# Kernel tuning notes

Hardware: AMD Instinct MI355X
Metric: run time of the kernel (lower is better)

Reference implementation:

```python
import math
import jax, jax.numpy as jnp
import numpy as np

L_LAYERS, H, D, DV, DM, LMAX, V = 4, 16, 1024, 64, 4096, 1024, 32000


def setup_inputs() -> dict:
    key = jax.random.key(0)
    ks = iter(jax.random.split(key, 40))
    def rn(shape, s=0.02):
        return jax.random.normal(next(ks), shape, jnp.float32) * s
    x_ids = jax.random.randint(next(ks), (LMAX,), 0, V)
    return dict(
        x_ids=x_ids,
        word_emb=rn((V, D)), pos_emb=rn((LMAX, D)),
        Wq=rn((L_LAYERS, H, D, D)), bq=jnp.zeros((L_LAYERS, H, D), jnp.float32),
        Wk=rn((L_LAYERS, H, D, D)), bk=jnp.zeros((L_LAYERS, H, D), jnp.float32),
        Wv=rn((L_LAYERS, H, D, DV)), bv=jnp.zeros((L_LAYERS, H, DV), jnp.float32),
        Wo=rn((L_LAYERS, H * DV, D)), bo=jnp.zeros((L_LAYERS, D), jnp.float32),
        g1=rn((L_LAYERS, D), 0.01), b1=rn((L_LAYERS, D), 0.01),
        g2=rn((L_LAYERS, D), 0.01), b2=rn((L_LAYERS, D), 0.01),
        W1=rn((L_LAYERS, D, DM)), bm1=jnp.zeros((L_LAYERS, DM), jnp.float32),
        W2=rn((L_LAYERS, DM, D)), bm2=jnp.zeros((L_LAYERS, D), jnp.float32),
        gf=rn((D,), 0.01), bf=rn((D,), 0.01),
        Wu=rn((D, V)), bu=jnp.zeros((V,), jnp.float32),
    )


def _ln(x, g, b):
    # original normalizes each row over the full embedding vector (biased std)
    mu = jnp.mean(x, axis=-1, keepdims=True)
    sd = jnp.sqrt(jnp.mean((x - mu) ** 2, axis=-1, keepdims=True))
    return g * (x - mu) / sd + b


def reference(x_ids, word_emb, pos_emb, Wq, bq, Wk, bk, Wv, bv, Wo, bo,
              g1, b1, g2, b2, W1, bm1, W2, bm2, gf, bf, Wu, bu):
    x = word_emb[x_ids] + pos_emb[jnp.arange(LMAX)]          # (LMAX, D)
    mask = jnp.tril(jnp.ones((LMAX, LMAX), bool))
    scale = 1.0 / math.sqrt(D)                               # d_attn = d_e
    for l in range(L_LAYERS):
        xn = _ln(x, g1[l], b1[l])
        q = jnp.einsum('ld,hde->hle', xn, Wq[l]) + bq[l][:, None, :]
        k = jnp.einsum('ld,hde->hle', xn, Wk[l]) + bk[l][:, None, :]
        v = jnp.einsum('ld,hdv->hlv', xn, Wv[l]) + bv[l][:, None, :]
        s = jnp.einsum('hqe,hke->hqk', q, k)                 # (H, LMAX, LMAX)
        s = jnp.where(mask, s, -jnp.inf)
        a = jax.nn.softmax(s * scale, axis=-1)
        o = jnp.einsum('hqk,hkv->hqv', a, v)                 # (H, LMAX, DV)
        # faithful reproduction of MHAttention's OVERLAPPING slice writes:
        # head h writes columns [h, h+DV), later heads overwrite earlier ones
        y = jnp.zeros((LMAX, H * DV), x.dtype)
        for h in range(H):
            y = y.at[:, h:h + DV].set(o[h])
        x = x + y @ Wo[l] + bo[l]
        xn2 = _ln(x, g2[l], b2[l])
        # x + act_layer(xn2) where act_layer(z) = z + mlp2(gelu(mlp1(z)))
        x = x + xn2 + jax.nn.gelu(xn2 @ W1[l] + bm1[l]) @ W2[l] + bm2[l]
    x = _ln(x, gf, bf)
    return jax.nn.softmax(x @ Wu + bu, axis=-1)              # (LMAX, V)
```

## Files before the change

kernel.cpp:

```cpp
#include <hip/hip_runtime.h>

typedef __bf16 bf16_t;
typedef __bf16 bf16x8 __attribute__((ext_vector_type(8)));
typedef float f32x4 __attribute__((ext_vector_type(4)));
typedef unsigned int u32;

#define SEQ    1024
#define DEMB   1024
#define NHEAD  16
#define DVDIM  64
#define DMLP   4096
#define NVOCAB 32000
#define NLAYER 4

typedef const __attribute__((address_space(1))) void gas_t;
typedef __attribute__((address_space(3))) void las_t;

__device__ __forceinline__ void gload_lds16(const void* g, void* l) {
  __builtin_amdgcn_global_load_lds((gas_t*)g, (las_t*)l, 16, 0, 0);
}

union PackU { bf16_t h[2]; u32 u; };
union B4U  { uint2 u; bf16_t h[4]; };

__device__ __forceinline__ float blockSum(float v, float* red) {
  #pragma unroll
  for (int o = 32; o > 0; o >>= 1) v += __shfl_down(v, o, 64);
  __syncthreads();
  if ((threadIdx.x & 63) == 0) red[threadIdx.x >> 6] = v;
  __syncthreads();
  return (red[0] + red[1]) + (red[2] + red[3]);
}
__device__ __forceinline__ float blockMax(float v, float* red) {
  #pragma unroll
  for (int o = 32; o > 0; o >>= 1) v = fmaxf(v, __shfl_down(v, o, 64));
  __syncthreads();
  if ((threadIdx.x & 63) == 0) red[threadIdx.x >> 6] = v;
  __syncthreads();
  return fmaxf(fmaxf(red[0], red[1]), fmaxf(red[2], red[3]));
}

__device__ __forceinline__ void ln_body(float4 v, const float* __restrict__ g,
                                        const float* __restrict__ b,
                                        bf16_t* __restrict__ xn, int row, int t,
                                        float* red, float* xupd_row) {
  float mu = blockSum(v.x + v.y + v.z + v.w, red) * (1.0f / DEMB);
  float dx = v.x - mu, dy = v.y - mu, dz = v.z - mu, dw = v.w - mu;
  float var = blockSum(dx * dx + dy * dy + dz * dz + dw * dw, red) * (1.0f / DEMB);
  float inv = 1.0f / sqrtf(var);
  float4 gv = *(const float4*)(g + t * 4);
  float4 bv = *(const float4*)(b + t * 4);
  float o0 = gv.x * dx * inv + bv.x;
  float o1 = gv.y * dy * inv + bv.y;
  float o2 = gv.z * dz * inv + bv.z;
  float o3 = gv.w * dw * inv + bv.w;
  PackU p0, p1;
  p0.h[0] = (bf16_t)o0; p0.h[1] = (bf16_t)o1;
  p1.h[0] = (bf16_t)o2; p1.h[1] = (bf16_t)o3;
  uint2 st; st.x = p0.u; st.y = p1.u;
  *(uint2*)(xn + (long)row * DEMB + t * 4) = st;
  if (xupd_row) {
    float4 nv; nv.x = v.x + o0; nv.y = v.y + o1; nv.z = v.z + o2; nv.w = v.w + o3;
    *(float4*)(xupd_row + t * 4) = nv;
  }
}

__global__ void __launch_bounds__(256)
embedln_k(const int* __restrict__ ids, const float* __restrict__ we,
          const float* __restrict__ pe, const float* __restrict__ g,
          const float* __restrict__ b, float* __restrict__ x,
          bf16_t* __restrict__ xn) {
  __shared__ float red[4];
  const int row = blockIdx.x, t = threadIdx.x;
  const long id = ids[row];
  float4 a = *(const float4*)(we + id * (long)DEMB + t * 4);
  float4 p = *(const float4*)(pe + (long)row * DEMB + t * 4);
  float4 v; v.x = a.x + p.x; v.y = a.y + p.y; v.z = a.z + p.z; v.w = a.w + p.w;
  *(float4*)(x + (long)row * DEMB + t * 4) = v;
  ln_body(v, g, b, xn, row, t, red, nullptr);
}

__global__ void __launch_bounds__(256)
ln_k(const float* __restrict__ x, const float* __restrict__ g,
     const float* __restrict__ b, bf16_t* __restrict__ xn,
     float* __restrict__ xupd) {
  __shared__ float red[4];
  const int row = blockIdx.x, t = threadIdx.x;
  float4 v = *(const float4*)(x + (long)row * DEMB + t * 4);
  ln_body(v, g, b, xn, row, t, red, xupd ? xupd + (long)row * DEMB : nullptr);
}

__global__ void __launch_bounds__(256)
redln_k(const float* __restrict__ P, const float* __restrict__ bm2,
        float* __restrict__ X, const float* __restrict__ g,
        const float* __restrict__ b, bf16_t* __restrict__ xn) {
  __shared__ float red[4];
  const int row = blockIdx.x, t = threadIdx.x;
  const long i = (long)row * 1024 + t * 4;
  float4 x = *(float4*)(X + i);
  #pragma unroll
  for (int z = 0; z < 4; ++z) {
    float4 p = *(const float4*)(P + (long)z * 1048576 + i);
    x.x += p.x; x.y += p.y; x.z += p.z; x.w += p.w;
  }
  float4 bb = *(const float4*)(bm2 + t * 4);
  x.x += bb.x; x.y += bb.y; x.z += bb.z; x.w += bb.w;
  *(float4*)(X + i) = x;
  ln_body(x, g, b, xn, row, t, red, nullptr);
}

__global__ void biaszyb_k(const float* __restrict__ bq, const float* __restrict__ bk,
                          float* __restrict__ out, bf16_t* __restrict__ y) {
  const int z = blockIdx.x, t = threadIdx.x;
  if (z < 128) {
    const int l = z >> 5, i = z & 31;
    const float* src = (i < NHEAD) ? (bq + (long)(l * NHEAD + i) * DEMB)
                                   : (bk + (long)(l * NHEAD + i - NHEAD) * DEMB);
    *(float4*)(out + (long)z * DEMB + t * 4) = *(const float4*)(src + t * 4);
  } else {
    *(uint4*)((char*)y + ((long)(z - 128) * 256 + t) * 16) = uint4{0, 0, 0, 0};
  }
}

__device__ __forceinline__ void tconv_tile(const float* __restrict__ ip,
                                           bf16_t* __restrict__ op,
                                           int R, int C, int rx, int ry,
                                           float (*tf)[65]) {
  const int c0 = rx * 64, r0 = ry * 128;
  const int t = threadIdx.x;
  #pragma unroll
  for (int p = 0; p < 8; ++p) {
    const int i = p * 256 + t;
    const int r = i >> 4, c4 = (i & 15) * 4;
    const float4 v = *(const float4*)(ip + (long)(r0 + r) * C + (c0 + c4));
    *(float4*)&tf[r][c4] = v;
  }
  __syncthreads();
  const int nn = t >> 2;
  const int seg = t & 3;
  #pragma unroll
  for (int q2 = 0; q2 < 4; ++q2) {
    u32 w[4];
    #pragma unroll
    for (int q = 0; q < 4; ++q) {
      const int row = seg * 32 + q2 * 8 + 2 * q;
      PackU u;
      u.h[0] = (bf16_t)tf[row][nn];
      u.h[1] = (bf16_t)tf[row + 1][nn];
      w[q] = u.u;
    }
    *(uint4*)(op + (long)(c0 + nn) * R + (r0 + seg * 32 + q2 * 8)) = *(uint4*)&w[0];
  }
}

__global__ void __launch_bounds__(256)
tconvall_k(const float* __restrict__ Wq, const float* __restrict__ Wk,
           const float* __restrict__ Wv, const float* __restrict__ Wo,
           const float* __restrict__ W1, const float* __restrict__ W2,
           const float* __restrict__ Wu,
           bf16_t* __restrict__ WTqk, bf16_t* __restrict__ WTv,
           bf16_t* __restrict__ WTo, bf16_t* __restrict__ WT1,
           bf16_t* __restrict__ WT2, bf16_t* __restrict__ WTu) {
  __shared__ float tf[128][65];
  const long DD = (long)DEMB * DEMB;
  const int b = blockIdx.x;
  const float* ip; bf16_t* op; int R, C, rx, ry;
  if (b < 16384) {
    const int z = b >> 7, rem = b & 127; ry = rem >> 4; rx = rem & 15;
    R = 1024; C = 1024;
    const int l = z >> 5, i = z & 31;
    ip = (i < NHEAD) ? (Wq + (long)(l * NHEAD + i) * DD)
                     : (Wk + (long)(l * NHEAD + i - NHEAD) * DD);
    op = WTqk + (long)z * DD;
  } else if (b < 16896) {
    const int idx = b - 16384; const int z = idx >> 3; ry = idx & 7; rx = 0;
    R = 1024; C = 64;
    ip = Wv + (long)z * 65536; op = WTv + (long)z * 65536;
  } else if (b < 16960) {
    const int idx = b - 16896; const int z = idx >> 4; ry = 0; rx = idx & 15;
    R = 128; C = 1024;
    ip = Wo + (long)z * DD; op = WTo + (long)z * 131072;
  } else if (b < 19008) {
    const int idx = b - 16960; const int z = idx >> 9, rem = idx & 511;
    ry = rem >> 6; rx = rem & 63;
    R = 1024; C = 4096;
    ip = W1 + (long)z * 4194304; op = WT1 + (long)z * 4194304;
  } else if (b < 21056) {
    const int idx = b - 19008; const int z = idx >> 9, rem = idx & 511;
    ry = rem >> 4; rx = rem & 15;
    R = 4096; C = 1024;
    ip = W2 + (long)z * 4194304; op = WT2 + (long)z * 4194304;
  } else {
    const int idx = b - 21056; ry = idx / 500; rx = idx - ry * 500;
    R = 1024; C = 32000;
    ip = Wu; op = WTu;
  }
  tconv_tile(ip, op, R, C, rx, ry, tf);
}

template<int MODE, int BN, bool CAUSAL, bool TRIMK>
__global__ void __launch_bounds__(256)
gemm_k(const bf16_t* __restrict__ A, const bf16_t* __restrict__ B,
       const float* __restrict__ bias, void* __restrict__ Cv,
       int M, int N, int K, int lda, int ldb,
       long aB, long bB, long cB, int biasB) {
  __shared__ bf16_t lsA[128 * 32];
  __shared__ bf16_t lsB[BN * 32];

  const int t = threadIdx.x;
  const int bz = blockIdx.z;
  const int m0 = blockIdx.y * 128;
  const int n0 = blockIdx.x * BN;
  if (CAUSAL && n0 > m0 + 127) return;

  const bf16_t* Ap = A + (long)bz * aB;
  const bf16_t* Bp = B + (long)bz * bB;
  const int kEnd = TRIMK ? min(K, m0 + 128) : K;

  constexpr int NS = BN / 32;
  const int lane = t & 63;
  const int wid = t >> 6;
  const int wr = (wid >> 1) * 64;
  const int wc = (wid & 1) * (BN / 2);
  const int fr = lane & 15, fg = lane >> 4;
  const int srow = lane >> 2;
  const int skc  = (lane & 3) * 8;

  f32x4 acc[4][NS] = {};

  for (int k0 = 0; k0 < kEnd; k0 += 32) {
    if (k0) __syncthreads();
    #pragma unroll
    for (int i = 0; i < 2; ++i) {
      const int seg = wid * 2 + i;
      gload_lds16(Ap + (long)(m0 + seg * 16 + srow) * lda + (k0 + skc),
                  lsA + seg * 512);
    }
    if (BN == 128) {
      #pragma unroll
      for (int i = 0; i < 2; ++i) {
        const int seg = wid * 2 + i;
        gload_lds16(Bp + (long)(n0 + seg * 16 + srow) * ldb + (k0 + skc),
                    lsB + seg * 512);
      }
    } else {
      gload_lds16(Bp + (long)(n0 + wid * 16 + srow) * ldb + (k0 + skc),
                  lsB + wid * 512);
    }
    __syncthreads();

    bf16x8 af[4], bfv[NS];
    #pragma unroll
    for (int ms = 0; ms < 4; ++ms)
      af[ms] = *(const bf16x8*)(lsA + (wr + ms * 16 + fr) * 32 + fg * 8);
    #pragma unroll
    for (int ns = 0; ns < NS; ++ns)
      bfv[ns] = *(const bf16x8*)(lsB + (wc + ns * 16 + fr) * 32 + fg * 8);
    #pragma unroll
    for (int ms = 0; ms < 4; ++ms)
      #pragma unroll
      for (int ns = 0; ns < NS; ++ns)
        acc[ms][ns] = __builtin_amdgcn_mfma_f32_16x16x32_bf16(
            af[ms], bfv[ns], acc[ms][ns], 0, 0, 0);
  }

  #pragma unroll
  for (int ms = 0; ms < 4; ++ms) {
    #pragma unroll
    for (int ns = 0; ns < NS; ++ns) {
      const int col = n0 + wc + ns * 16 + fr;
      const float bvv = bias ? bias[(long)bz * biasB + col] : 0.0f;
      #pragma unroll
      for (int r = 0; r < 4; ++r) {
        const int row = m0 + wr + ms * 16 + fg * 4 + r;
        float v = acc[ms][ns][r] + bvv;
        if (MODE == 1) {
          ((float*)Cv)[(long)bz * cB + (long)row * N + col] += v;
        } else if (MODE == 2) {
          ((float*)Cv)[(long)bz * cB + (long)row * N + col] = v;
        } else {
          float gl = 0.5f * v * (1.0f + tanhf(0.7978845608028654f * (v + 0.044715f * v * v * v)));
          ((bf16_t*)Cv)[(long)bz * cB + (long)row * N + col] = (bf16_t)gl;
        }
      }
    }
  }
}

#define GPHASE(buf, mh, nh, STAGE, VM) do {                                            \
  bf16x8 af[4][2], bfv[2][2];                                                          \
  _Pragma("unroll") for (int mf = 0; mf < 4; ++mf) {                                   \
    const int r = wm * 128 + ((mh) * 4 + mf) * 16 + (lane & 15);                       \
    _Pragma("unroll") for (int ks = 0; ks < 2; ++ks) {                                 \
      const int slot = ks * 4 + (lane >> 4);                                           \
      af[mf][ks] = *(const bf16x8*)(lds + (buf) * 32768 + r * 64 +                     \
                                    ((slot ^ (r & 7)) << 3)); } }                      \
  _Pragma("unroll") for (int nf = 0; nf < 2; ++nf) {                                   \
    const int r = wn * 64 + ((nh) * 2 + nf) * 16 + (lane & 15);                        \
    _Pragma("unroll") for (int ks = 0; ks < 2; ++ks) {                                 \
      const int slot = ks * 4 + (lane >> 4);                                           \
      bfv[nf][ks] = *(const bf16x8*)(lds + (buf) * 32768 + 16384 + r * 64 +            \
                                     ((slot ^ (r & 7)) << 3)); } }                     \
  STAGE;                                                                               \
  __builtin_amdgcn_s_barrier();                                                        \
  asm volatile("s_waitcnt lgkmcnt(0)" ::: "memory");                                   \
  __builtin_amdgcn_sched_barrier(0);                                                   \
  __builtin_amdgcn_s_setprio(1);                                                       \
  _Pragma("unroll") for (int mf = 0; mf < 4; ++mf)                                     \
    _Pragma("unroll") for (int nf = 0; nf < 2; ++nf)                                   \
      _Pragma("unroll") for (int ks = 0; ks < 2; ++ks)                                 \
        acc[(mh) * 4 + mf][(nh) * 2 + nf] = __builtin_amdgcn_mfma_f32_16x16x32_bf16(   \
            af[mf][ks], bfv[nf][ks], acc[(mh) * 4 + mf][(nh) * 2 + nf], 0, 0, 0);      \
  __builtin_amdgcn_s_setprio(0);                                                       \
  VM;                                                                                  \
  __builtin_amdgcn_s_barrier();                                                        \
} while (0)

template<int MODE, bool CAUSAL, int VZ>
__global__ void __launch_bounds__(512, 1)
gemm256_k(const bf16_t* __restrict__ A, const bf16_t* __restrict__ B,
          const float* __restrict__ bias, void* __restrict__ Cv,
          int M, int N, int K, long aB, long bB, long cB, int biasB,
          const bf16_t* __restrict__ A2, const bf16_t* __restrict__ B2,
          const float* __restrict__ bias2, bf16_t* __restrict__ Cv2) {
  __shared__ bf16_t lds[65536];

  const int t = threadIdx.x;
  const int lane = t & 63, w = t >> 6;
  const int wm = w >> 2, wn = w & 3;
  const int bz = blockIdx.z;
  const int m0 = blockIdx.y * 256, n0 = blockIdx.x * 256;
  const bool vm = (VZ >= 0) && (bz == VZ);
  if (CAUSAL && !vm && n0 > m0 + 255) return;

  const bf16_t* Ap = vm ? A2 : A + (long)bz * aB;
  const bf16_t* Bp = vm ? B2 : B + (long)bz * bB;
  const int NT = K >> 6;

  f32x4 acc[8][4] = {};

  auto stA = [&](int half, int kt, int buf) {
    #pragma unroll
    for (int rr = 0; rr < 2; ++rr) {
      const int rw0 = rr * 64 + w * 8;
      const int row0 = ((rw0 >> 6) << 7) | (half << 6) | (rw0 & 63);
      const int r = row0 + (lane >> 3);
      const int slot = lane & 7;
      gload_lds16(Ap + (long)(m0 + r) * K + (kt << 6) + ((slot ^ (r & 7)) << 3),
                  lds + buf * 32768 + row0 * 64);
    }
  };
  auto stB = [&](int half, int kt, int buf) {
    #pragma unroll
    for (int rr = 0; rr < 2; ++rr) {
      const int rw0 = rr * 64 + w * 8;
      const int row0 = ((rw0 >> 5) << 6) | (half << 5) | (rw0 & 31);
      const int r = row0 + (lane >> 3);
      const int slot = lane & 7;
      gload_lds16(Bp + (long)(n0 + r) * K + (kt << 6) + ((slot ^ (r & 7)) << 3),
                  lds + buf * 32768 + 16384 + row0 * 64);
    }
  };

  stB(0, 0, 0); stA(0, 0, 0); stA(1, 0, 0); stB(1, 0, 0);
  stB(0, 1, 1); stA(0, 1, 1);
  asm volatile("s_waitcnt vmcnt(4)" ::: "memory");
  __builtin_amdgcn_s_barrier();

  for (int it = 0; it < (NT >> 1); ++it) {
    const int tt = it * 2;
    const int s1 = min(tt + 1, NT - 1);
    const int s2 = min(tt + 2, NT - 1);
    const int s3 = min(tt + 3, NT - 1);
    GPHASE(0, 0, 0, { stA(1, s1, 1); }, );
    GPHASE(0, 1, 0, { stB(1, s1, 1); }, );
    GPHASE(0, 0, 1, { stB(0, s2, 0); }, );
    GPHASE(0, 1, 1, { stA(0, s2, 0); }, asm volatile("s_waitcnt vmcnt(4)" ::: "memory"));
    GPHASE(1, 0, 0, { stA(1, s2, 0); }, );
    GPHASE(1, 1, 0, { stB(1, s2, 0); }, );
    GPHASE(1, 0, 1, { stB(0, s3, 1); }, );
    GPHASE(1, 1, 1, { stA(0, s3, 1); }, asm volatile("s_waitcnt vmcnt(4)" ::: "memory"));
  }
  asm volatile("s_waitcnt vmcnt(0)" ::: "memory");

  #pragma unroll
  for (int mf = 0; mf < 8; ++mf) {
    #pragma unroll
    for (int nf = 0; nf < 4; ++nf) {
      const int col = n0 + wn * 64 + nf * 16 + (lane & 15);
      const int row0 = m0 + wm * 128 + mf * 16 + (lane >> 4) * 4;
      if (vm) {
        const float bvv = bias2[col];
        PackU p0, p1;
        p0.h[0] = (bf16_t)(acc[mf][nf][0] + bvv);
        p0.h[1] = (bf16_t)(acc[mf][nf][1] + bvv);
        p1.h[0] = (bf16_t)(acc[mf][nf][2] + bvv);
        p1.h[1] = (bf16_t)(acc[mf][nf][3] + bvv);
        uint2 st; st.x = p0.u; st.y = p1.u;
        *(uint2*)(Cv2 + (long)col * M + row0) = st;
      } else {
        const float bvv = bias ? bias[(long)bz * biasB + col] : 0.0f;
        #pragma unroll
        for (int r = 0; r < 4; ++r) {
          const float v = acc[mf][nf][r] + bvv;
          if (MODE == 0)
            ((bf16_t*)Cv)[(long)bz * cB + (long)(row0 + r) * N + col] = (bf16_t)v;
          else
            ((float*)Cv)[(long)bz * cB + (long)(row0 + r) * N + col] = v;
        }
      }
    }
  }
}

__global__ void __launch_bounds__(256)
smax_k(const bf16_t* __restrict__ s, const bf16_t* __restrict__ V,
       bf16_t* __restrict__ Yb) {
  __shared__ float red[4];
  __shared__ float pl[1024];
  __shared__ float rcol[4][64];
  const int q = blockIdx.x, h = blockIdx.y, t = threadIdx.x;
  const bf16_t* sr = s + ((long)h * SEQ + q) * SEQ;
  const int L = q + 1;
  const float scale = 0.03125f;
  B4U b; b.u = *(const uint2*)(sr + t * 4);
  float x[4];
  float m = -1e30f;
  #pragma unroll
  for (int j = 0; j < 4; ++j) {
    x[j] = (float)b.h[j] * scale;
    if (t * 4 + j < L) m = fmaxf(m, x[j]);
  }
  m = blockMax(m, red);
  float e[4], sum = 0.0f;
  #pragma unroll
  for (int j = 0; j < 4; ++j) {
    e[j] = (t * 4 + j < L) ? expf(x[j] - m) : 0.0f;
    sum += e[j];
  }
  __syncthreads();
  sum = blockSum(sum, red);
  const float inv = 1.0f / sum;
  if (h != NHEAD - 1) {
    const bf16_t* vc = V + (long)h * 64 * SEQ;
    B4U vv; vv.u = *(const uint2*)(vc + t * 4);
    float d = 0.0f;
    #pragma unroll
    for (int j = 0; j < 4; ++j) d += e[j] * (float)vv.h[j];
    __syncthreads();
    d = blockSum(d, red);
    if (t == 0) Yb[(long)q * 128 + h] = (bf16_t)(d * inv);
  } else {
    #pragma unroll
    for (int j = 0; j < 4; ++j) pl[t * 4 + j] = e[j];
    __syncthreads();
    const int c = t & 63, grp = t >> 6;
    const bf16_t* vr = V + ((long)(NHEAD - 1) * 64 + c) * SEQ + grp * 256;
    float part = 0.0f;
    #pragma unroll
    for (int kk = 0; kk < 256; kk += 8) {
      bf16x8 v8 = *(const bf16x8*)(vr + kk);
      #pragma unroll
      for (int j = 0; j < 8; ++j) part += pl[grp * 256 + kk + j] * (float)v8[j];
    }
    rcol[grp][c] = part;
    __syncthreads();
    if (t < 64) {
      const float d = rcol[0][t] + rcol[1][t] + rcol[2][t] + rcol[3][t];
      Yb[(long)q * 128 + 15 + t] = (bf16_t)(d * inv);
    }
  }
}

__global__ void __launch_bounds__(1024)
vsmax_k(float* __restrict__ out) {
  __shared__ float rm[16], rs[16];
  const int row = blockIdx.x, t = threadIdx.x;
  float* r = out + (long)row * NVOCAB;
  float v[32];
  const int nlast = (t < NVOCAB - 31 * 1024) ? 32 : 31;
  float m = -1e30f;
  #pragma unroll
  for (int j = 0; j < 31; ++j) { v[j] = r[j * 1024 + t]; m = fmaxf(m, v[j]); }
  if (nlast == 32) { v[31] = r[31 * 1024 + t]; m = fmaxf(m, v[31]); } else v[31] = -1e30f;
  float s = 0.0f;
  #pragma unroll
  for (int j = 0; j < 32; ++j) s += expf(v[j] - m);
  #pragma unroll
  for (int o = 32; o > 0; o >>= 1) {
    const float mo = __shfl_down(m, o, 64);
    const float so = __shfl_down(s, o, 64);
    const float M2 = fmaxf(m, mo);
    s = s * expf(m - M2) + so * expf(mo - M2);
    m = M2;
  }
  if ((t & 63) == 0) { rm[t >> 6] = m; rs[t >> 6] = s; }
  __syncthreads();
  float M = -1e30f;
  #pragma unroll
  for (int i = 0; i < 16; ++i) M = fmaxf(M, rm[i]);
  float S = 0.0f;
  #pragma unroll
  for (int i = 0; i < 16; ++i) S += rs[i] * expf(rm[i] - M);
  const float inv = 1.0f / S;
  #pragma unroll
  for (int j = 0; j < 31; ++j) r[j * 1024 + t] = expf(v[j] - M) * inv;
  if (nlast == 32) r[31 * 1024 + t] = expf(v[31] - M) * inv;
}

extern "C" void kernel_launch(void* const* d_in, const int* in_sizes, int n_in,
                              void* d_out, int out_size, void* d_ws, size_t ws_size,
                              hipStream_t stream) {
  (void)in_sizes; (void)n_in; (void)out_size; (void)ws_size;
  const int*   x_ids = (const int*)  d_in[0];
  const float* wemb  = (const float*)d_in[1];
  const float* pemb  = (const float*)d_in[2];
  const float* Wq    = (const float*)d_in[3];
  const float* bq    = (const float*)d_in[4];
  const float* Wk    = (const float*)d_in[5];
  const float* bk    = (const float*)d_in[6];
  const float* Wv    = (const float*)d_in[7];
  const float* bv    = (const float*)d_in[8];
  const float* Wo    = (const float*)d_in[9];
  const float* bo    = (const float*)d_in[10];
  const float* g1    = (const float*)d_in[11];
  const float* b1    = (const float*)d_in[12];
  const float* g2    = (const float*)d_in[13];
  const float* b2    = (const float*)d_in[14];
  const float* W1    = (const float*)d_in[15];
  const float* bm1   = (const float*)d_in[16];
  const float* W2    = (const float*)d_in[17];
  const float* bm2   = (const float*)d_in[18];
  const float* gf    = (const float*)d_in[19];
  const float* bfin  = (const float*)d_in[20];
  const float* Wu    = (const float*)d_in[21];
  const float* bu    = (const float*)d_in[22];

  char* ws = (char*)d_ws;
  float*  X    = (float*) ws;
  bf16_t* ACT  = (bf16_t*)(ws + (4u   << 20));
  bf16_t* VbT  = (bf16_t*)(ws + (6u   << 20));
  bf16_t* Yb   = (bf16_t*)(ws + (10u  << 20));
  bf16_t* H1   = (bf16_t*)(ws + (12u  << 20));
  bf16_t* QKb  = (bf16_t*)(ws + (20u  << 20));
  float*  PART = (float*) (ws + (84u  << 20));
  float*  BIAS = (float*) (ws + (100u << 20));
  bf16_t* WTqk = (bf16_t*)(ws + (128u << 20));
  bf16_t* WTv  = (bf16_t*)(ws + (384u << 20));
  bf16_t* WTo  = (bf16_t*)(ws + (392u << 20));
  bf16_t* WT1  = (bf16_t*)(ws + (400u << 20));
  bf16_t* WT2  = (bf16_t*)(ws + (432u << 20));
  bf16_t* WTu  = (bf16_t*)(ws + (464u << 20));

  bf16_t* Sb  = (bf16_t*)d_out;
  float*  OUT = (float*)d_out;

  const long DD = (long)DEMB * DEMB;
  const long SD = (long)SEQ * DEMB;

  embedln_k<<<SEQ, 256, 0, stream>>>(x_ids, wemb, pemb, g1, b1, X, ACT);
  biaszyb_k<<<192, 256, 0, stream>>>(bq, bk, BIAS, Yb);
  tconvall_k<<<25056, 256, 0, stream>>>(Wq, Wk, Wv, Wo, W1, W2, Wu,
                                        WTqk, WTv, WTo, WT1, WT2, WTu);

  for (int l = 0; l < NLAYER; ++l) {
    gemm256_k<0, false, -1><<<dim3(4, 4, 32), 512, 0, stream>>>(
        ACT, WTqk + (long)l * 32 * DD, BIAS + (long)l * 32 * DEMB, QKb,
        SEQ, DEMB, DEMB, 0L, DD, SD, DEMB,
        nullptr, nullptr, nullptr, nullptr);

    gemm256_k<0, true, NHEAD><<<dim3(4, 4, NHEAD + 1), 512, 0, stream>>>(
        QKb, QKb + (long)NHEAD * SD, nullptr, Sb,
        SEQ, SEQ, DEMB, SD, SD, (long)SEQ * SEQ, 0,
        ACT, WTv + (long)l * DD, bv + (long)l * NHEAD * DVDIM, VbT);

    smax_k<<<dim3(SEQ, NHEAD), 256, 0, stream>>>(Sb, VbT, Yb);

    gemm_k<1, 64, false, false><<<dim3(16, 8, 1), 256, 0, stream>>>(
        Yb, WTo + (long)l * DEMB * 128, bo + (long)l * DEMB, X,
        SEQ, DEMB, 128, 128, 128, 0L, 0L, 0L, 0);

    ln_k<<<SEQ, 256, 0, stream>>>(X, g2 + l * DEMB, b2 + l * DEMB, ACT, X);

    gemm_k<3, 128, false, false><<<dim3(32, 8, 1), 256, 0, stream>>>(
        ACT, WT1 + (long)l * DMLP * DEMB, bm1 + (long)l * DMLP, H1,
        SEQ, DMLP, DEMB, DEMB, DEMB, 0L, 0L, 0L, 0);
    gemm_k<2, 128, false, false><<<dim3(8, 8, 4), 256, 0, stream>>>(
        H1, WT2 + (long)l * DEMB * DMLP, nullptr, PART,
        SEQ, DEMB, 1024, DMLP, DMLP, 1024L, 1024L, (long)SEQ * DEMB, 0);
    if (l < NLAYER - 1)
      redln_k<<<SEQ, 256, 0, stream>>>(PART, bm2 + (long)l * DEMB, X,
                                       g1 + (l + 1) * DEMB, b1 + (l + 1) * DEMB, ACT);
    else
      redln_k<<<SEQ, 256, 0, stream>>>(PART, bm2 + (long)l * DEMB, X, gf, bfin, ACT);
  }

  gemm256_k<2, false, -1><<<dim3(125, 4, 1), 512, 0, stream>>>(
      ACT, WTu, bu, OUT, SEQ, NVOCAB, DEMB, 0L, 0L, 0L, 0,
      nullptr, nullptr, nullptr, nullptr);
  vsmax_k<<<SEQ, 1024, 0, stream>>>(OUT);
}
```

Before: 1.512 ms.

## Pack causal score GEMM grid and make softmax one-wave-per-row

The causal QK^T GEMM now launches a packed 1D grid of 176 blocks: 16 blocks for the V projection plus only the lower-triangular tiles for each head. This replaces the 4x4x17 grid in which upper-triangle blocks exited early. The softmax kernel now handles four query rows per block, one wavefront per row, and does its reductions with shuffles instead of block-wide LDS reductions and barriers. The last-head path computes all 64 columns from shared probabilities per row. The transpose kernel also reorders its store indices so adjacent threads write consecutive segments, aiming for better coalescing. The risk is lower parallelism in the last-head path, where each thread loops over all 1024 keys.

```diff
diff --git a/kernel.cpp b/kernel.cpp
--- a/kernel.cpp
+++ b/kernel.cpp
@@ -137,19 +137,19 @@
   }
   __syncthreads();
   const int nn = t >> 2;
-  const int seg = t & 3;
+  const int sub = t & 3;
   #pragma unroll
   for (int q2 = 0; q2 < 4; ++q2) {
+    const int base = q2 * 32 + sub * 8;
     u32 w[4];
     #pragma unroll
     for (int q = 0; q < 4; ++q) {
-      const int row = seg * 32 + q2 * 8 + 2 * q;
       PackU u;
-      u.h[0] = (bf16_t)tf[row][nn];
-      u.h[1] = (bf16_t)tf[row + 1][nn];
+      u.h[0] = (bf16_t)tf[base + 2 * q][nn];
+      u.h[1] = (bf16_t)tf[base + 2 * q + 1][nn];
       w[q] = u.u;
     }
-    *(uint4*)(op + (long)(c0 + nn) * R + (r0 + seg * 32 + q2 * 8)) = *(uint4*)&w[0];
+    *(uint4*)(op + (long)(c0 + nn) * R + (r0 + base)) = *(uint4*)&w[0];
   }
 }
 
@@ -316,7 +316,7 @@
   __builtin_amdgcn_s_barrier();                                                        \
 } while (0)
 
-template<int MODE, bool CAUSAL, int VZ>
+template<int MODE, bool CAUSAL, int VZ, bool PACKED>
 __global__ void __launch_bounds__(512, 1)
 gemm256_k(const bf16_t* __restrict__ A, const bf16_t* __restrict__ B,
           const float* __restrict__ bias, void* __restrict__ Cv,
@@ -328,13 +328,29 @@
   const int t = threadIdx.x;
   const int lane = t & 63, w = t >> 6;
   const int wm = w >> 2, wn = w & 3;
-  const int bz = blockIdx.z;
-  const int m0 = blockIdx.y * 256, n0 = blockIdx.x * 256;
-  const bool vm = (VZ >= 0) && (bz == VZ);
-  if (CAUSAL && !vm && n0 > m0 + 255) return;
-
-  const bf16_t* Ap = vm ? A2 : A + (long)bz * aB;
-  const bf16_t* Bp = vm ? B2 : B + (long)bz * bB;
+  int m0, n0, zz; bool vm;
+  if (PACKED) {
+    const int id = blockIdx.x;
+    if (id < 16) {
+      vm = true; zz = 0;
+      m0 = (id >> 2) * 256; n0 = (id & 3) * 256;
+    } else {
+      vm = false;
+      const int idd = id - 16;
+      zz = idd & 15;
+      const int pi = idd >> 4;
+      const int by = (pi >= 1) + (pi >= 3) + (pi >= 6);
+      const int bx = pi - (by * (by + 1)) / 2;
+      m0 = by * 256; n0 = bx * 256;
+    }
+  } else {
+    zz = blockIdx.z; m0 = blockIdx.y * 256; n0 = blockIdx.x * 256;
+    vm = (VZ >= 0) && (zz == VZ);
+    if (CAUSAL && !vm && n0 > m0 + 255) return;
+  }
+
+  const bf16_t* Ap = vm ? A2 : A + (long)zz * aB;
+  const bf16_t* Bp = vm ? B2 : B + (long)zz * bB;
   const int NT = K >> 6;
 
   f32x4 acc[8][4] = {};
@@ -399,14 +415,14 @@
         uint2 st; st.x = p0.u; st.y = p1.u;
         *(uint2*)(Cv2 + (long)col * M + row0) = st;
       } else {
-        const float bvv = bias ? bias[(long)bz * biasB + col] : 0.0f;
+        const float bvv = bias ? bias[(long)zz * biasB + col] : 0.0f;
         #pragma unroll
         for (int r = 0; r < 4; ++r) {
           const float v = acc[mf][nf][r] + bvv;
           if (MODE == 0)
-            ((bf16_t*)Cv)[(long)bz * cB + (long)(row0 + r) * N + col] = (bf16_t)v;
+            ((bf16_t*)Cv)[(long)zz * cB + (long)(row0 + r) * N + col] = (bf16_t)v;
           else
-            ((float*)Cv)[(long)bz * cB + (long)(row0 + r) * N + col] = v;
+            ((float*)Cv)[(long)zz * cB + (long)(row0 + r) * N + col] = v;
         }
       }
     }
@@ -416,59 +432,68 @@
 __global__ void __launch_bounds__(256)
 smax_k(const bf16_t* __restrict__ s, const bf16_t* __restrict__ V,
        bf16_t* __restrict__ Yb) {
-  __shared__ float red[4];
-  __shared__ float pl[1024];
-  __shared__ float rcol[4][64];
-  const int q = blockIdx.x, h = blockIdx.y, t = threadIdx.x;
+  __shared__ float pl[4][1024];
+  const int qb = blockIdx.x, h = blockIdx.y, t = threadIdx.x;
+  const int w = t >> 6, lane = t & 63;
+  const int q = qb * 4 + w;
   const bf16_t* sr = s + ((long)h * SEQ + q) * SEQ;
   const int L = q + 1;
   const float scale = 0.03125f;
-  B4U b; b.u = *(const uint2*)(sr + t * 4);
-  float x[4];
+  float e[16];
   float m = -1e30f;
   #pragma unroll
-  for (int j = 0; j < 4; ++j) {
-    x[j] = (float)b.h[j] * scale;
-    if (t * 4 + j < L) m = fmaxf(m, x[j]);
-  }
-  m = blockMax(m, red);
-  float e[4], sum = 0.0f;
-  #pragma unroll
-  for (int j = 0; j < 4; ++j) {
-    e[j] = (t * 4 + j < L) ? expf(x[j] - m) : 0.0f;
-    sum += e[j];
-  }
-  __syncthreads();
-  sum = blockSum(sum, red);
+  for (int c = 0; c < 4; ++c) {
+    B4U bb; bb.u = *(const uint2*)(sr + lane * 16 + c * 4);
+    #pragma unroll
+    for (int j = 0; j < 4; ++j) {
+      const float x = (float)bb.h[j] * scale;
+      e[c * 4 + j] = x;
+      if (lane * 16 + c * 4 + j < L) m = fmaxf(m, x);
+    }
+  }
+  #pragma unroll
+  for (int o = 32; o > 0; o >>= 1) m = fmaxf(m, __shfl_xor(m, o, 64));
+  float sum = 0.0f;
+  #pragma unroll
+  for (int i = 0; i < 16; ++i) {
+    e[i] = (lane * 16 + i < L) ? expf(e[i] - m) : 0.0f;
+    sum += e[i];
+  }
+  #pragma unroll
+  for (int o = 32; o > 0; o >>= 1) sum += __shfl_xor(sum, o, 64);
   const float inv = 1.0f / sum;
+
   if (h != NHEAD - 1) {
-    const bf16_t* vc = V + (long)h * 64 * SEQ;
-    B4U vv; vv.u = *(const uint2*)(vc + t * 4);
+    const bf16_t* vc = V + (long)h * 64 * SEQ + lane * 16;
     float d = 0.0f;
     #pragma unroll
-    for (int j = 0; j < 4; ++j) d += e[j] * (float)vv.h[j];
+    for (int c = 0; c < 4; ++c) {
+      B4U vv; vv.u = *(const uint2*)(vc + c * 4);
+      #pragma unroll
+      for (int j = 0; j < 4; ++j) d += e[c * 4 + j] * (float)vv.h[j];
+    }
+    #pragma unroll
+    for (int o = 32; o > 0; o >>= 1) d += __shfl_xor(d, o, 64);
+    if (lane == 0) Yb[(long)q * 128 + h] = (bf16_t)(d * inv);
+  } else {
+    #pragma unroll
+    for (int c = 0; c < 4; ++c)
+      *(float4*)&pl[w][lane * 16 + c * 4] = *(float4*)&e[c * 4];
     __syncthreads();
-    d = blockSum(d, red);
-    if (t == 0) Yb[(long)q * 128 + h] = (bf16_t)(d * inv);
-  } else {
-    #pragma unroll
-    for (int j = 0; j < 4; ++j) pl[t * 4 + j] = e[j];
-    __syncthreads();
-    const int c = t & 63, grp = t >> 6;
-    const bf16_t* vr = V + ((long)(NHEAD - 1) * 64 + c) * SEQ + grp * 256;
-    float part = 0.0f;
-    #pragma unroll
-    for (int kk = 0; kk < 256; kk += 8) {
+    const int c = t & 63, r = t >> 6;
+    const int qq = qb * 4 + r;
+    const bf16_t* vr = V + ((long)(NHEAD - 1) * 64 + c) * SEQ;
+    float d = 0.0f;
+    for (int kk = 0; kk < 1024; kk += 8) {
       bf16x8 v8 = *(const bf16x8*)(vr + kk);
       #pragma unroll
-      for (int j = 0; j < 8; ++j) part += pl[grp * 256 + kk + j] * (float)v8[j];
-    }
-    rcol[grp][c] = part;
-    __syncthreads();
-    if (t < 64) {
-      const float d = rcol[0][t] + rcol[1][t] + rcol[2][t] + rcol[3][t];
-      Yb[(long)q * 128 + 15 + t] = (bf16_t)(d * inv);
-    }
+      for (int j = 0; j < 8; ++j) d += pl[r][kk + j] * (float)v8[j];
+    }
+    float sr2 = 0.0f;
+    for (int kk = t & 63; kk < 1024; kk += 64) sr2 += pl[r][kk];
+    #pragma unroll
+    for (int o = 32; o > 0; o >>= 1) sr2 += __shfl_xor(sr2, o, 64);
+    Yb[(long)qq * 128 + 15 + c] = (bf16_t)(d / sr2);
   }
 }
 
@@ -564,17 +589,17 @@
                                         WTqk, WTv, WTo, WT1, WT2, WTu);
 
   for (int l = 0; l < NLAYER; ++l) {
-    gemm256_k<0, false, -1><<<dim3(4, 4, 32), 512, 0, stream>>>(
+    gemm256_k<0, false, -1, false><<<dim3(4, 4, 32), 512, 0, stream>>>(
         ACT, WTqk + (long)l * 32 * DD, BIAS + (long)l * 32 * DEMB, QKb,
         SEQ, DEMB, DEMB, 0L, DD, SD, DEMB,
         nullptr, nullptr, nullptr, nullptr);
 
-    gemm256_k<0, true, NHEAD><<<dim3(4, 4, NHEAD + 1), 512, 0, stream>>>(
+    gemm256_k<0, true, 0, true><<<dim3(176), 512, 0, stream>>>(
         QKb, QKb + (long)NHEAD * SD, nullptr, Sb,
         SEQ, SEQ, DEMB, SD, SD, (long)SEQ * SEQ, 0,
         ACT, WTv + (long)l * DD, bv + (long)l * NHEAD * DVDIM, VbT);
 
-    smax_k<<<dim3(SEQ, NHEAD), 256, 0, stream>>>(Sb, VbT, Yb);
+    smax_k<<<dim3(SEQ / 4, NHEAD), 256, 0, stream>>>(Sb, VbT, Yb);
 
     gemm_k<1, 64, false, false><<<dim3(16, 8, 1), 256, 0, stream>>>(
         Yb, WTo + (long)l * DEMB * 128, bo + (long)l * DEMB, X,
@@ -595,7 +620,7 @@
       redln_k<<<SEQ, 256, 0, stream>>>(PART, bm2 + (long)l * DEMB, X, gf, bfin, ACT);
   }
 
-  gemm256_k<2, false, -1><<<dim3(125, 4, 1), 512, 0, stream>>>(
+  gemm256_k<2, false, -1, false><<<dim3(125, 4, 1), 512, 0, stream>>>(
       ACT, WTu, bu, OUT, SEQ, NVOCAB, DEMB, 0L, 0L, 0L, 0,
       nullptr, nullptr, nullptr, nullptr);
   vsmax_k<<<SEQ, 1024, 0, stream>>>(OUT);
```

Result: faster. 1.393 ms (-7.9%).
